# Kernel optimization log

Hardware: AMD Instinct MI355X
Metric: run time of the kernel (lower is better)

The kernel has to match this reference:

```python
import jax, jax.numpy as jnp
import numpy as np

N = 50000       # nodes
E = 1_600_000   # edges (avg degree 32)
LAT, HID, OUT = 64, 128, 64


def _add_self_loops(edge_index, edge_attr, n):
    loop = jnp.arange(n, dtype=edge_index.dtype)
    src = jnp.concatenate([edge_index[0], loop])
    dst = jnp.concatenate([edge_index[1], loop])
    ew = jnp.concatenate([edge_attr, jnp.ones((n,), edge_attr.dtype)])
    return src, dst, ew


def _gcn_conv(x, W, b, src, dst, ew, n):
    # x: [N, Fin] -> [N, Fout]; GCN: D^{-1/2}(A+I)D^{-1/2} X W + b
    h = x @ W                                             # [N, Fout]
    deg = jax.ops.segment_sum(ew, dst, num_segments=n)    # weighted in-degree
    dinv = jnp.where(deg > 0, jax.lax.rsqrt(deg), 0.0)
    norm = dinv[src] * ew * dinv[dst]                     # [E+N]
    out = jax.ops.segment_sum(norm[:, None] * h[src], dst, num_segments=n)
    return out + b


def setup_inputs() -> dict:
    key = jax.random.key(0)
    k = jax.random.split(key, 8)
    z = jax.random.normal(k[0], (N, LAT), jnp.float32)
    edge_index = jax.random.randint(k[1], (2, E), 0, N, dtype=jnp.int32)
    edge_attr = jax.random.uniform(k[2], (E,), jnp.float32)
    W1 = jax.random.normal(k[3], (LAT, HID), jnp.float32) / np.sqrt(LAT)
    b1 = jnp.zeros((HID,), jnp.float32)
    W2 = jax.random.normal(k[4], (HID, OUT), jnp.float32) / np.sqrt(HID)
    b2 = jnp.zeros((OUT,), jnp.float32)
    return {"z": z, "edge_index": edge_index, "edge_attr": edge_attr,
            "W1": W1, "b1": b1, "W2": W2, "b2": b2}


def reference(z, edge_index, edge_attr, W1, b1, W2, b2):
    n = z.shape[0]
    src, dst, ew = _add_self_loops(edge_index, edge_attr, n)
    hidden = jax.nn.relu(_gcn_conv(z, W1, b1, src, dst, ew, n))
    return _gcn_conv(hidden, W2, b2, src, dst, ew, n)
```

## Files before the change

### kernel.cpp

```cpp
#include <hip/hip_runtime.h>


#define NPB 64
#define CH  4096

typedef __attribute__((ext_vector_type(8))) short short8v;
typedef __attribute__((ext_vector_type(4))) float f32x4;

__device__ __forceinline__ float4 ld4(const float* p) {
    return *reinterpret_cast<const float4*>(p);
}

__device__ __forceinline__ unsigned bfr(float f) {
    unsigned u = __float_as_uint(f);
    return (u + 0x7FFFu + ((u >> 16) & 1u)) >> 16;
}
__device__ __forceinline__ void bf2(unsigned v, float& lo, float& hi) {
    lo = __uint_as_float(v << 16);
    hi = __uint_as_float(v & 0xFFFF0000u);
}

__device__ __forceinline__ void scan_btot(const int* __restrict__ btot, int NBKT,
                                          int* bbs, int* wtot) {
    int tid = threadIdx.x;
    int v[4];
    int s = 0;
#pragma unroll
    for (int q = 0; q < 4; ++q) {
        int i = 4 * tid + q;
        v[q] = (i < NBKT) ? btot[i] : 0;
        s += v[q];
    }
    int lane = tid & 63, wid = tid >> 6;
    int incl = s;
#pragma unroll
    for (int off = 1; off < 64; off <<= 1) {
        int u = __shfl_up(incl, off, 64);
        if (lane >= off) incl += u;
    }
    if (lane == 63) wtot[wid] = incl;
    __syncthreads();
    int woff = 0;
#pragma unroll
    for (int w = 0; w < 4; ++w) if (w < wid) woff += wtot[w];
    int ex = woff + incl - s;
#pragma unroll
    for (int q = 0; q < 4; ++q) {
        int i = 4 * tid + q;
        if (i < NBKT) bbs[i] = ex;
        ex += v[q];
    }
    __syncthreads();
}

__global__ __launch_bounds__(256) void hist_kernel(const int* __restrict__ dst,
                                                   int* __restrict__ hist,
                                                   int E, int G1, int NBKT) {
    __shared__ int lh[1024];
    for (int i = threadIdx.x; i < NBKT; i += 256) lh[i] = 0;
    __syncthreads();
    int g = blockIdx.x;
    int beg = g * CH, end = min(beg + CH, E);
    for (int j = beg + (int)threadIdx.x; j < end; j += 256)
        atomicAdd(&lh[dst[j] / NPB], 1);
    __syncthreads();
    for (int i = threadIdx.x; i < NBKT; i += 256) hist[(size_t)i * G1 + g] = lh[i];
}

__global__ __launch_bounds__(64) void bscan_kernel(int* __restrict__ hist,
                                                   int* __restrict__ btot, int G1) {
    int b = blockIdx.x;
    int* row = hist + (size_t)b * G1;
    int lane = threadIdx.x;
    int carry = 0;
    for (int g0 = 0; g0 < G1; g0 += 64) {
        int g = g0 + lane;
        int v = (g < G1) ? row[g] : 0;
        int incl = v;
#pragma unroll
        for (int off = 1; off < 64; off <<= 1) {
            int u = __shfl_up(incl, off, 64);
            if (lane >= off) incl += u;
        }
        if (g < G1) row[g] = carry + incl - v;
        carry += __shfl(incl, 63, 64);
    }
    if (lane == 0) btot[b] = carry;
}

__global__ __launch_bounds__(256) void scatter_kernel(const int* __restrict__ src,
                                                      const int* __restrict__ dst,
                                                      const float* __restrict__ ew,
                                                      const int* __restrict__ hist,
                                                      const int* __restrict__ btot,
                                                      int2* __restrict__ tmp,
                                                      int E, int G1, int NBKT) {
    __shared__ int bbs[1024];
    __shared__ int wtot[4];
    __shared__ int cursor[1024];
    scan_btot(btot, NBKT, bbs, wtot);
    int g = blockIdx.x;
    for (int i = threadIdx.x; i < NBKT; i += 256)
        cursor[i] = bbs[i] + hist[(size_t)i * G1 + g];
    __syncthreads();
    int beg = g * CH, end = min(beg + CH, E);
    for (int j = beg + (int)threadIdx.x; j < end; j += 256) {
        int d = dst[j];
        int b = d / NPB;
        int pos = atomicAdd(&cursor[b], 1);
        tmp[pos] = make_int2(((d & (NPB - 1)) << 24) | src[j], __float_as_int(ew[j]));
    }
}

__global__ __launch_bounds__(256) void finalize_kernel(const int2* __restrict__ tmp,
                                                       const int* __restrict__ btot,
                                                       const float* __restrict__ z,
                                                       int* __restrict__ rowptr,
                                                       float* __restrict__ dinv,
                                                       unsigned* __restrict__ csr,
                                                       uint2* __restrict__ zs,
                                                       int n, int E, int NBKT) {
    __shared__ int bbs[1024];
    __shared__ int wsum_[4];
    __shared__ unsigned int hist[NPB];
    __shared__ float dvl[NPB];
    scan_btot(btot, NBKT, bbs, wsum_);
    int b = blockIdx.x;
    int base = bbs[b];
    int cnt  = btot[b];
    int tid  = threadIdx.x;
    if (tid < NPB) hist[tid] = 0;
    __syncthreads();
    for (int j = tid; j < cnt; j += 256) {
        int2 t = tmp[base + j];
        unsigned dlow = ((unsigned)t.x) >> 24;
        unsigned wfix = (unsigned)(__int_as_float(t.y) * 16384.0f);
        atomicAdd(&hist[dlow], (1u << 24) | wfix);
    }
    __syncthreads();
    if (tid < NPB) {
        unsigned pk = hist[tid];
        int c = (int)(pk >> 24);
        int incl = c;
#pragma unroll
        for (int off = 1; off < 64; off <<= 1) {
            int u = __shfl_up(incl, off, 64);
            if (tid >= off) incl += u;
        }
        int excl = incl - c;
        int node = b * NPB + tid;
        float dv = 0.f;
        if (node < n) {
            rowptr[node] = base + excl;
            float wdeg = (float)(pk & 0xFFFFFFu) * (1.0f / 16384.0f);
            dv = rsqrtf(wdeg + 1.0f);
            dinv[node] = dv;
        }
        dvl[tid]  = dv;
        hist[tid] = (unsigned)excl;
    }
    if (b == 0 && tid == 0) rowptr[n] = E;
    __syncthreads();
    for (int j = tid; j < cnt; j += 256) {
        int2 t = tmp[base + j];
        unsigned dlow = ((unsigned)t.x) >> 24;
        unsigned srcv = (unsigned)(t.x & 0xFFFFFF);
        int lr = (int)atomicAdd(&hist[dlow], 1u);
        csr[base + lr] = srcv | (bfr(__int_as_float(t.y)) << 16);
    }
    for (int t = tid; t < NPB * 16; t += 256) {
        int li = t >> 4;
        int node = b * NPB + li;
        if (node < n) {
            int k = t & 15;
            float dv = dvl[li];
            float4 f = ld4(z + (size_t)node * 64 + k * 4);
            zs[(size_t)node * 16 + k] =
                make_uint2(bfr(dv * f.x) | (bfr(dv * f.y) << 16),
                           bfr(dv * f.z) | (bfr(dv * f.w) << 16));
        }
    }
}

template<bool BIAS, bool OUTB>
__global__ __launch_bounds__(256) void gaggb_kernel(const int* __restrict__ rowptr,
                                                    const unsigned* __restrict__ csr,
                                                    const float* __restrict__ dinv,
                                                    const uint4* __restrict__ Hp4,
                                                    const float* __restrict__ b,
                                                    void* __restrict__ out, int n) {
    int row  = (blockIdx.x * 256 + threadIdx.x) >> 6;
    int lane = threadIdx.x & 63;
    if (row >= n) return;
    int eg = lane >> 3, fq = lane & 7;
    int beg = rowptr[row], end = rowptr[row + 1];
    float dv = dinv[row];

    float a0 = 0.f, a1 = 0.f, a2 = 0.f, a3 = 0.f;
    float a4 = 0.f, a5 = 0.f, a6 = 0.f, a7 = 0.f;
    float f0, f1, f2, f3, f4, f5, f6, f7;

#define ACCUM(V, W)                                            \
    bf2((V).x, f0, f1); bf2((V).y, f2, f3);                    \
    bf2((V).z, f4, f5); bf2((V).w, f6, f7);                    \
    a0 += (W) * f0; a1 += (W) * f1; a2 += (W) * f2; a3 += (W) * f3; \
    a4 += (W) * f4; a5 += (W) * f5; a6 += (W) * f6; a7 += (W) * f7;

    int j = beg;
    for (; j + 32 <= end; j += 32) {
        unsigned m0 = csr[j + eg];
        unsigned m1 = csr[j + eg + 8];
        unsigned m2 = csr[j + eg + 16];
        unsigned m3 = csr[j + eg + 24];
        uint4 v0 = Hp4[(size_t)(m0 & 0xFFFFu) * 8 + fq];
        uint4 v1 = Hp4[(size_t)(m1 & 0xFFFFu) * 8 + fq];
        uint4 v2 = Hp4[(size_t)(m2 & 0xFFFFu) * 8 + fq];
        uint4 v3 = Hp4[(size_t)(m3 & 0xFFFFu) * 8 + fq];
        float w0 = __uint_as_float(m0 & 0xFFFF0000u);
        float w1 = __uint_as_float(m1 & 0xFFFF0000u);
        float w2 = __uint_as_float(m2 & 0xFFFF0000u);
        float w3 = __uint_as_float(m3 & 0xFFFF0000u);
        ACCUM(v0, w0) ACCUM(v1, w1) ACCUM(v2, w2) ACCUM(v3, w3)
    }
    for (; j + 8 <= end; j += 8) {
        unsigned m0 = csr[j + eg];
        float w0 = __uint_as_float(m0 & 0xFFFF0000u);
        uint4 v0 = Hp4[(size_t)(m0 & 0xFFFFu) * 8 + fq];
        ACCUM(v0, w0)
    }
    if (j < end) {
        int idx = j + eg;
        if (idx < end) {
            unsigned m0 = csr[idx];
            float w0 = __uint_as_float(m0 & 0xFFFF0000u);
            uint4 v0 = Hp4[(size_t)(m0 & 0xFFFFu) * 8 + fq];
            ACCUM(v0, w0)
        }
    }
#undef ACCUM
#pragma unroll
    for (int off = 8; off < 64; off <<= 1) {
        a0 += __shfl_xor(a0, off, 64); a1 += __shfl_xor(a1, off, 64);
        a2 += __shfl_xor(a2, off, 64); a3 += __shfl_xor(a3, off, 64);
        a4 += __shfl_xor(a4, off, 64); a5 += __shfl_xor(a5, off, 64);
        a6 += __shfl_xor(a6, off, 64); a7 += __shfl_xor(a7, off, 64);
    }

    if (eg == 0) {
        uint4 sv = Hp4[(size_t)row * 8 + fq];
        float s0, s1, s2, s3, s4, s5, s6, s7;
        bf2(sv.x, s0, s1); bf2(sv.y, s2, s3);
        bf2(sv.z, s4, s5); bf2(sv.w, s6, s7);
        float o0 = dv * (a0 + s0), o1 = dv * (a1 + s1);
        float o2 = dv * (a2 + s2), o3 = dv * (a3 + s3);
        float o4 = dv * (a4 + s4), o5 = dv * (a5 + s5);
        float o6 = dv * (a6 + s6), o7 = dv * (a7 + s7);
        if (BIAS) {
            float4 b0 = ld4(b + fq * 8);
            float4 b1v = ld4(b + fq * 8 + 4);
            o0 += b0.x; o1 += b0.y; o2 += b0.z; o3 += b0.w;
            o4 += b1v.x; o5 += b1v.y; o6 += b1v.z; o7 += b1v.w;
        }
        if (OUTB) {
            uint4 pv = make_uint4(bfr(o0) | (bfr(o1) << 16),
                                  bfr(o2) | (bfr(o3) << 16),
                                  bfr(o4) | (bfr(o5) << 16),
                                  bfr(o6) | (bfr(o7) << 16));
            reinterpret_cast<uint4*>(out)[(size_t)row * 8 + fq] = pv;
        } else {
            float4* op = reinterpret_cast<float4*>((float*)out + (size_t)row * 64 + fq * 8);
            op[0] = make_float4(o0, o1, o2, o3);
            op[1] = make_float4(o4, o5, o6, o7);
        }
    }
}

__global__ __launch_bounds__(256) void densemfma_kernel(
        const unsigned short* __restrict__ t1b,
        const float* __restrict__ W1,
        const float* __restrict__ b1,
        const float* __restrict__ W2,
        const float* __restrict__ dinv,
        unsigned short* __restrict__ hs,
        int n) {
    __shared__ __align__(16) unsigned short W1s[128][68];
    __shared__ __align__(16) unsigned short W2s[64][132];
    __shared__ float b1s[128];
    __shared__ __align__(16) unsigned short hT[4][16][136];
    for (int i = threadIdx.x; i < 128 * 64; i += 256) {
        int c = i >> 6, k = i & 63;
        W1s[c][k] = (unsigned short)bfr(W1[k * 128 + c]);
    }
    for (int i = threadIdx.x; i < 64 * 128; i += 256) {
        int c = i >> 7, k = i & 127;
        W2s[c][k] = (unsigned short)bfr(W2[k * 64 + c]);
    }
    if (threadIdx.x < 128) b1s[threadIdx.x] = b1[threadIdx.x];
    __syncthreads();

    int wv = threadIdx.x >> 6;
    int l  = threadIdx.x & 63;
    int m  = l & 15, g = l >> 4;
    int ngrp = (n + 63) >> 6;
    for (int grp = blockIdx.x; grp < ngrp; grp += gridDim.x) {
        int R = grp * 64 + wv * 16;
        short8v a0 = {0,0,0,0,0,0,0,0}, a1 = {0,0,0,0,0,0,0,0};
        int rowA = R + m;
        if (rowA < n) {
            a0 = *reinterpret_cast<const short8v*>(t1b + (size_t)rowA * 64 + 8 * g);
            a1 = *reinterpret_cast<const short8v*>(t1b + (size_t)rowA * 64 + 32 + 8 * g);
        }
#pragma unroll
        for (int ct = 0; ct < 8; ++ct) {
            short8v wb0 = *reinterpret_cast<const short8v*>(&W1s[ct * 16 + m][8 * g]);
            short8v wb1 = *reinterpret_cast<const short8v*>(&W1s[ct * 16 + m][32 + 8 * g]);
            f32x4 c = {0.f, 0.f, 0.f, 0.f};
            c = __builtin_amdgcn_mfma_f32_16x16x32_bf16(a0, wb0, c, 0, 0, 0);
            c = __builtin_amdgcn_mfma_f32_16x16x32_bf16(a1, wb1, c, 0, 0, 0);
            float bb = b1s[ct * 16 + m];
#pragma unroll
            for (int r = 0; r < 4; ++r) {
                float v = fmaxf(c[r] + bb, 0.f);
                hT[wv][4 * g + r][ct * 16 + m] = (unsigned short)bfr(v);
            }
        }
        f32x4 acc2[4];
#pragma unroll
        for (int ct = 0; ct < 4; ++ct) acc2[ct] = (f32x4){0.f, 0.f, 0.f, 0.f};
#pragma unroll
        for (int kk = 0; kk < 4; ++kk) {
            short8v ha = *reinterpret_cast<const short8v*>(&hT[wv][m][kk * 32 + 8 * g]);
#pragma unroll
            for (int ct = 0; ct < 4; ++ct) {
                short8v wb = *reinterpret_cast<const short8v*>(
                    &W2s[ct * 16 + m][kk * 32 + 8 * g]);
                acc2[ct] = __builtin_amdgcn_mfma_f32_16x16x32_bf16(ha, wb, acc2[ct], 0, 0, 0);
            }
        }
#pragma unroll
        for (int r = 0; r < 4; ++r) {
            int grow = R + 4 * g + r;
            float dv = (grow < n) ? dinv[grow] : 0.f;
#pragma unroll
            for (int ct = 0; ct < 4; ++ct)
                hT[wv][4 * g + r][ct * 16 + m] = (unsigned short)bfr(acc2[ct][r] * dv);
        }
        int growO = R + m;
        if (growO < n) {
            uint4 u0 = *reinterpret_cast<const uint4*>(&hT[wv][m][g * 16]);
            uint4 u1 = *reinterpret_cast<const uint4*>(&hT[wv][m][g * 16 + 8]);
            *reinterpret_cast<uint4*>(hs + (size_t)growO * 64 + g * 16) = u0;
            *reinterpret_cast<uint4*>(hs + (size_t)growO * 64 + g * 16 + 8) = u1;
        }
    }
}

extern "C" void kernel_launch(void* const* d_in, const int* in_sizes, int n_in,
                              void* d_out, int out_size, void* d_ws, size_t ws_size,
                              hipStream_t stream) {
    const float* z  = (const float*)d_in[0];
    const int*   ei = (const int*)d_in[1];
    const float* ea = (const float*)d_in[2];
    const float* W1 = (const float*)d_in[3];
    const float* b1 = (const float*)d_in[4];
    const float* W2 = (const float*)d_in[5];
    const float* b2 = (const float*)d_in[6];
    float* out = (float*)d_out;

    const int n = in_sizes[0] / 64;
    const int E = in_sizes[2];
    const int* src = ei;
    const int* dst = ei + E;
    const int NBKT = (n + NPB - 1) / NPB;
    const int G1   = (E + CH - 1) / CH;

    float* ws = (float*)d_ws;
    size_t p = 0;
    auto alloc = [&](size_t elems) { size_t o = p; p += (elems + 63) & ~63ull; return o; };
    float*    dinv   = ws + alloc(n);
    int*      rowptr = (int*)(ws + alloc((size_t)n + 1));
    int*      btot   = (int*)(ws + alloc(NBKT));
    unsigned* csr    = (unsigned*)(ws + alloc(E));
    unsigned short* t1b = (unsigned short*)(ws + alloc((size_t)n * 32));
    uint2*    zs     = (uint2*)(ws + alloc((size_t)n * 32));
    float*    X      = ws + alloc((size_t)E * 2 + (size_t)NBKT * G1 + 64);
    int2*     tmp    = (int2*)X;
    int*      hist   = (int*)(X + (size_t)E * 2);
    (void)ws_size;

    hist_kernel<<<G1, 256, 0, stream>>>(dst, hist, E, G1, NBKT);
    bscan_kernel<<<NBKT, 64, 0, stream>>>(hist, btot, G1);
    scatter_kernel<<<G1, 256, 0, stream>>>(src, dst, ea, hist, btot, tmp, E, G1, NBKT);
    finalize_kernel<<<NBKT, 256, 0, stream>>>(tmp, btot, z, rowptr, dinv,
                                              csr, zs, n, E, NBKT);

    const int gblocks = (n + 3) / 4;
    gaggb_kernel<false, true><<<gblocks, 256, 0, stream>>>(rowptr, csr, dinv,
                                                           (const uint4*)zs,
                                                           nullptr, t1b, n);
    densemfma_kernel<<<256, 256, 0, stream>>>(t1b, W1, b1, W2, dinv,
                                              (unsigned short*)zs, n);
    gaggb_kernel<true, false><<<gblocks, 256, 0, stream>>>(rowptr, csr, dinv,
                                                           (const uint4*)zs,
                                                           b2, out, n);
}
```

Measured before the change: 137.6 us.

## Stage scatter edges in LDS by bucket for coalesced tmp writes

The scatter kernel now recounts per-bucket counts locally and scans them. It places each chunk's edges into a shared-memory staging buffer ordered by bucket, then writes them to the global temporary array in contiguous runs instead of scattered 8-byte stores. The block histogram layout is also transposed to chunk-major, so hist_kernel writes are coalesced while bscan reads become strided. The change costs an extra pass over dst, about 52KB of LDS per block (which lowers occupancy), and packs dst and src into 16 bits each, so it assumes n < 65536.

```diff
diff --git a/kernel.cpp b/kernel.cpp
--- a/kernel.cpp
+++ b/kernel.cpp
@@ -20,15 +20,15 @@
     hi = __uint_as_float(v & 0xFFFF0000u);
 }
 
-__device__ __forceinline__ void scan_btot(const int* __restrict__ btot, int NBKT,
-                                          int* bbs, int* wtot) {
+__device__ __forceinline__ void scan_any(const int* __restrict__ srcarr, int NBKT,
+                                         int* dstarr, int* wtot) {
     int tid = threadIdx.x;
     int v[4];
     int s = 0;
 #pragma unroll
     for (int q = 0; q < 4; ++q) {
         int i = 4 * tid + q;
-        v[q] = (i < NBKT) ? btot[i] : 0;
+        v[q] = (i < NBKT) ? srcarr[i] : 0;
         s += v[q];
     }
     int lane = tid & 63, wid = tid >> 6;
@@ -47,7 +47,7 @@
 #pragma unroll
     for (int q = 0; q < 4; ++q) {
         int i = 4 * tid + q;
-        if (i < NBKT) bbs[i] = ex;
+        if (i < NBKT) dstarr[i] = ex;
         ex += v[q];
     }
     __syncthreads();
@@ -64,25 +64,26 @@
     for (int j = beg + (int)threadIdx.x; j < end; j += 256)
         atomicAdd(&lh[dst[j] / NPB], 1);
     __syncthreads();
-    for (int i = threadIdx.x; i < NBKT; i += 256) hist[(size_t)i * G1 + g] = lh[i];
+    for (int i = threadIdx.x; i < NBKT; i += 256)
+        hist[(size_t)g * NBKT + i] = lh[i];
 }
 
 __global__ __launch_bounds__(64) void bscan_kernel(int* __restrict__ hist,
-                                                   int* __restrict__ btot, int G1) {
+                                                   int* __restrict__ btot,
+                                                   int G1, int NBKT) {
     int b = blockIdx.x;
-    int* row = hist + (size_t)b * G1;
     int lane = threadIdx.x;
     int carry = 0;
     for (int g0 = 0; g0 < G1; g0 += 64) {
         int g = g0 + lane;
-        int v = (g < G1) ? row[g] : 0;
+        int v = (g < G1) ? hist[(size_t)g * NBKT + b] : 0;
         int incl = v;
 #pragma unroll
         for (int off = 1; off < 64; off <<= 1) {
             int u = __shfl_up(incl, off, 64);
             if (lane >= off) incl += u;
         }
-        if (g < G1) row[g] = carry + incl - v;
+        if (g < G1) hist[(size_t)g * NBKT + b] = carry + incl - v;
         carry += __shfl(incl, 63, 64);
     }
     if (lane == 0) btot[b] = carry;
@@ -97,18 +98,40 @@
                                                       int E, int G1, int NBKT) {
     __shared__ int bbs[1024];
     __shared__ int wtot[4];
+    __shared__ int lcount[1024];
+    __shared__ int lbase[1024];
     __shared__ int cursor[1024];
-    scan_btot(btot, NBKT, bbs, wtot);
+    __shared__ int gbase[1024];
+    __shared__ int2 stg[CH];
+    int tid = threadIdx.x;
+    scan_any(btot, NBKT, bbs, wtot);
     int g = blockIdx.x;
-    for (int i = threadIdx.x; i < NBKT; i += 256)
-        cursor[i] = bbs[i] + hist[(size_t)i * G1 + g];
-    __syncthreads();
-    int beg = g * CH, end = min(beg + CH, E);
-    for (int j = beg + (int)threadIdx.x; j < end; j += 256) {
+    for (int i = tid; i < NBKT; i += 256) lcount[i] = 0;
+    __syncthreads();
+    int beg = g * CH, end = min(beg + CH, E), cnt = end - beg;
+    for (int j = beg + tid; j < end; j += 256)
+        atomicAdd(&lcount[dst[j] / NPB], 1);
+    __syncthreads();
+    scan_any(lcount, NBKT, lbase, wtot);
+    for (int i = tid; i < NBKT; i += 256) {
+        cursor[i] = lbase[i];
+        gbase[i]  = bbs[i] + hist[(size_t)g * NBKT + i];
+    }
+    __syncthreads();
+    for (int j = beg + tid; j < end; j += 256) {
         int d = dst[j];
-        int b = d / NPB;
-        int pos = atomicAdd(&cursor[b], 1);
-        tmp[pos] = make_int2(((d & (NPB - 1)) << 24) | src[j], __float_as_int(ew[j]));
+        int pos = atomicAdd(&cursor[d / NPB], 1);
+        stg[pos] = make_int2((int)(((unsigned)d << 16) | (unsigned)src[j]),
+                             __float_as_int(ew[j]));
+    }
+    __syncthreads();
+    for (int i = tid; i < cnt; i += 256) {
+        int2 e = stg[i];
+        unsigned dx = (unsigned)e.x;
+        int b = (int)(dx >> 22);
+        int gpos = gbase[b] + (i - lbase[b]);
+        int dlow = (int)((dx >> 16) & 63);
+        tmp[gpos] = make_int2((dlow << 24) | (int)(dx & 0xFFFFu), e.y);
     }
 }
 
@@ -124,7 +147,7 @@
     __shared__ int wsum_[4];
     __shared__ unsigned int hist[NPB];
     __shared__ float dvl[NPB];
-    scan_btot(btot, NBKT, bbs, wsum_);
+    scan_any(btot, NBKT, bbs, wsum_);
     int b = blockIdx.x;
     int base = bbs[b];
     int cnt  = btot[b];
@@ -164,7 +187,7 @@
     for (int j = tid; j < cnt; j += 256) {
         int2 t = tmp[base + j];
         unsigned dlow = ((unsigned)t.x) >> 24;
-        unsigned srcv = (unsigned)(t.x & 0xFFFFFF);
+        unsigned srcv = (unsigned)(t.x & 0xFFFF);
         int lr = (int)atomicAdd(&hist[dlow], 1u);
         csr[base + lr] = srcv | (bfr(__int_as_float(t.y)) << 16);
     }
@@ -389,7 +412,7 @@
     (void)ws_size;
 
     hist_kernel<<<G1, 256, 0, stream>>>(dst, hist, E, G1, NBKT);
-    bscan_kernel<<<NBKT, 64, 0, stream>>>(hist, btot, G1);
+    bscan_kernel<<<NBKT, 64, 0, stream>>>(hist, btot, G1, NBKT);
     scatter_kernel<<<G1, 256, 0, stream>>>(src, dst, ea, hist, btot, tmp, E, G1, NBKT);
     finalize_kernel<<<NBKT, 256, 0, stream>>>(tmp, btot, z, rowptr, dinv,
                                               csr, zs, n, E, NBKT);
```

New measurement: 135.4 us. Within noise of the previous version (-1.6%).
